# Kernel optimization log

Measured on AMD Instinct MI355X. Metric: run time of the kernel, lower is better.

## Reference

```python
import jax, jax.numpy as jnp
import numpy as np

TAU = 0.1
EPS = 1e-8

def _l2norm(x, axis):
    # matches F.normalize: x / max(||x||, 1e-12)
    n = jnp.sqrt(jnp.sum(x * x, axis=axis, keepdims=True))
    return x / jnp.maximum(n, 1e-12)

def setup_inputs() -> dict:
    key = jax.random.key(0)
    k1, k2, k3 = jax.random.split(key, 3)
    B, D, K = 262144, 256, 64
    return {
        "features": jax.random.normal(k1, (B, D), dtype=jnp.float32),
        "prototypes": jax.random.normal(k2, (K, D), dtype=jnp.float32),
        "domain_labels": jax.random.randint(k3, (B,), 0, K, dtype=jnp.int64),
    }

def reference(features, prototypes, domain_labels):
    f = _l2norm(features, 1)            # (B, D)
    p = _l2norm(prototypes, 1)          # (K, D)
    sim = jnp.einsum('bd,kd->bk', f, p) / TAU   # (B, K)
    e = jnp.exp(sim)                    # (B, K)
    numerator = jnp.take_along_axis(e, domain_labels[:, None], axis=1)[:, 0]  # (B,)
    denominator = jnp.sum(e, axis=1)    # (B,)
    loss = -jnp.log((numerator + EPS) / (denominator + EPS) + EPS)
    return jnp.mean(loss)
```

## Files before the change

### kernel.cpp

```cpp
#include <hip/hip_runtime.h>
#include <stdint.h>

typedef __attribute__((ext_vector_type(8))) short short8;
typedef __attribute__((ext_vector_type(4))) float floatx4;

#define EPS 1e-8f
#define TAU 0.1f

__device__ __forceinline__ unsigned short f2bf(float f) {
  union { float f; unsigned u; } v; v.f = f;
  unsigned u = v.u;
  u += 0x7fffu + ((u >> 16) & 1u);
  return (unsigned short)(u >> 16);
}

__global__ void proto_prep(const float* __restrict__ protos,
                           unsigned short* __restrict__ pbf) {
  const int l = threadIdx.x & 63;
  const int w = threadIdx.x >> 6;
  const int row = blockIdx.x * 4 + w;
  float4 v = reinterpret_cast<const float4*>(protos)[row * 64 + l];
  float ss = v.x * v.x + v.y * v.y + v.z * v.z + v.w * v.w;
#pragma unroll
  for (int d = 1; d < 64; d <<= 1) ss += __shfl_xor(ss, d, 64);
  const float inv = 1.0f / fmaxf(sqrtf(ss), 1e-12f);
  ushort4 o;
  o.x = f2bf(v.x * inv); o.y = f2bf(v.y * inv);
  o.z = f2bf(v.z * inv); o.w = f2bf(v.w * inv);
  reinterpret_cast<ushort4*>(pbf)[row * 64 + l] = o;
}

__global__ void protonce_main(const float* __restrict__ feat,
                              const unsigned short* __restrict__ pbf,
                              const int* __restrict__ labels,
                              float* __restrict__ partials) {
  const int tid = threadIdx.x;
  const int l = tid & 63;
  const int w = tid >> 6;
  const int n = l & 15;
  const int q = l >> 4;
  const long rowBase = (long)blockIdx.x * 64 + w * 16;

  const float* arow = feat + (rowBase + n) * 256 + q * 8;
  float4 av[16];
#pragma unroll
  for (int s = 0; s < 8; ++s) {
    av[2 * s]     = *reinterpret_cast<const float4*>(arow + s * 32);
    av[2 * s + 1] = *reinterpret_cast<const float4*>(arow + s * 32 + 4);
  }

  float ss = 0.f;
  short8 af[8];
#pragma unroll
  for (int s = 0; s < 8; ++s) {
    float4 x = av[2 * s], y = av[2 * s + 1];
    ss += x.x * x.x + x.y * x.y + x.z * x.z + x.w * x.w +
          y.x * y.x + y.y * y.y + y.z * y.z + y.w * y.w;
    short8 t;
    t[0] = f2bf(x.x); t[1] = f2bf(x.y); t[2] = f2bf(x.z); t[3] = f2bf(x.w);
    t[4] = f2bf(y.x); t[5] = f2bf(y.y); t[6] = f2bf(y.z); t[7] = f2bf(y.w);
    af[s] = t;
  }
  ss += __shfl_xor(ss, 16, 64);
  ss += __shfl_xor(ss, 32, 64);

  floatx4 acc[4] = {{0.f, 0.f, 0.f, 0.f}, {0.f, 0.f, 0.f, 0.f},
                    {0.f, 0.f, 0.f, 0.f}, {0.f, 0.f, 0.f, 0.f}};
  const unsigned short* bbase = pbf + n * 256 + q * 8;
#pragma unroll
  for (int s = 0; s < 8; ++s) {
#pragma unroll
    for (int t = 0; t < 4; ++t) {
      short8 bf = *reinterpret_cast<const short8*>(bbase + t * 4096 + s * 32);
      acc[t] = __builtin_amdgcn_mfma_f32_16x16x32_bf16(af[s], bf, acc[t], 0, 0, 0);
    }
  }

  const int4 lv = *reinterpret_cast<const int4*>(labels + rowBase + q * 4);
  float lossAcc = 0.f;
#pragma unroll
  for (int r = 0; r < 4; ++r) {
    const int row = q * 4 + r;
    const float nrm = __shfl(ss, row, 64);
    const float sc = 1.0f / (fmaxf(sqrtf(nrm), 1e-12f) * TAU);
    const int lab = (r == 0) ? lv.x : (r == 1) ? lv.y : (r == 2) ? lv.z : lv.w;
    float den = 0.f, num = 0.f;
#pragma unroll
    for (int t = 0; t < 4; ++t) {
      const float e = __expf(acc[t][r] * sc);
      den += e;
      num += (t * 16 + n == lab) ? e : 0.f;
    }
#pragma unroll
    for (int d = 1; d < 16; d <<= 1) {
      den += __shfl_xor(den, d, 64);
      num += __shfl_xor(num, d, 64);
    }
    if (n == 0) lossAcc += -__logf((num + EPS) / (den + EPS) + EPS);
  }
  lossAcc += __shfl_xor(lossAcc, 16, 64);
  lossAcc += __shfl_xor(lossAcc, 32, 64);

  __shared__ float wsum[4];
  if (l == 0) wsum[w] = lossAcc;
  __syncthreads();
  if (tid == 0) partials[blockIdx.x] = wsum[0] + wsum[1] + wsum[2] + wsum[3];
}

__global__ void finalize_k(const float* __restrict__ partials, int nblocks,
                           float* __restrict__ out, float invB) {
  __shared__ float red[256];
  float s = 0.f;
  for (int i = threadIdx.x; i < nblocks; i += 256) s += partials[i];
  red[threadIdx.x] = s;
  __syncthreads();
#pragma unroll
  for (int d = 128; d > 0; d >>= 1) {
    if (threadIdx.x < d) red[threadIdx.x] += red[threadIdx.x + d];
    __syncthreads();
  }
  if (threadIdx.x == 0) out[0] = red[0] * invB;
}

extern "C" void kernel_launch(void* const* d_in, const int* in_sizes, int n_in,
                              void* d_out, int out_size, void* d_ws, size_t ws_size,
                              hipStream_t stream) {
  const float* feat = (const float*)d_in[0];
  const float* protos = (const float*)d_in[1];
  const int* labels = (const int*)d_in[2];
  float* out = (float*)d_out;
  const int Bn = in_sizes[0] / 256;
  const int nblocks = Bn / 64;
  unsigned short* pbf = (unsigned short*)d_ws;
  float* partials = (float*)((char*)d_ws + 64 * 256 * sizeof(unsigned short));

  hipLaunchKernelGGL(proto_prep, dim3(16), dim3(256), 0, stream, protos, pbf);
  hipLaunchKernelGGL(protonce_main, dim3(nblocks), dim3(256), 0, stream,
                     feat, pbf, labels, partials);
  hipLaunchKernelGGL(finalize_k, dim3(1), dim3(256), 0, stream, partials,
                     nblocks, out, 1.0f / (float)Bn);
}
```

Baseline: 383.8 us.

## Stream feature loads through MFMA loop with truncating bf16 pack and launch bounds

The feature row is now loaded in two halves: the second half is fetched while the first half is converted and fed to the MFMAs. This cuts live registers, and launch_bounds(256,4) asks for higher occupancy. The round-to-nearest bf16 conversion is replaced by a single byte-permute truncation per pair of floats, which lowers ALU cost but slightly changes rounding of the feature operands. The kernel is memory-bound on a 256 MB feature read, so the main aim is more waves in flight to hide load latency.

Result: no change. 377.4 us (-1.7%).

```diff
diff --git a/kernel.cpp b/kernel.cpp
--- a/kernel.cpp
+++ b/kernel.cpp
@@ -12,6 +12,11 @@
   unsigned u = v.u;
   u += 0x7fffu + ((u >> 16) & 1u);
   return (unsigned short)(u >> 16);
+}
+
+__device__ __forceinline__ unsigned pack2_trunc(float lo, float hi) {
+  union { float f; unsigned u; } a, b; a.f = lo; b.f = hi;
+  return __builtin_amdgcn_perm(b.u, a.u, 0x07060302u);
 }
 
 __global__ void proto_prep(const float* __restrict__ protos,
@@ -30,10 +35,11 @@
   reinterpret_cast<ushort4*>(pbf)[row * 64 + l] = o;
 }
 
-__global__ void protonce_main(const float* __restrict__ feat,
-                              const unsigned short* __restrict__ pbf,
-                              const int* __restrict__ labels,
-                              float* __restrict__ partials) {
+__global__ __launch_bounds__(256, 4)
+void protonce_main(const float* __restrict__ feat,
+                   const unsigned short* __restrict__ pbf,
+                   const int* __restrict__ labels,
+                   float* __restrict__ partials) {
   const int tid = threadIdx.x;
   const int l = tid & 63;
   const int w = tid >> 6;
@@ -42,39 +48,42 @@
   const long rowBase = (long)blockIdx.x * 64 + w * 16;
 
   const float* arow = feat + (rowBase + n) * 256 + q * 8;
-  float4 av[16];
+  const unsigned short* bbase = pbf + n * 256 + q * 8;
+
+  float4 avx[4], avy[4];
 #pragma unroll
-  for (int s = 0; s < 8; ++s) {
-    av[2 * s]     = *reinterpret_cast<const float4*>(arow + s * 32);
-    av[2 * s + 1] = *reinterpret_cast<const float4*>(arow + s * 32 + 4);
+  for (int i = 0; i < 4; ++i) {
+    avx[i] = *reinterpret_cast<const float4*>(arow + i * 32);
+    avy[i] = *reinterpret_cast<const float4*>(arow + i * 32 + 4);
   }
-
-  float ss = 0.f;
-  short8 af[8];
-#pragma unroll
-  for (int s = 0; s < 8; ++s) {
-    float4 x = av[2 * s], y = av[2 * s + 1];
-    ss += x.x * x.x + x.y * x.y + x.z * x.z + x.w * x.w +
-          y.x * y.x + y.y * y.y + y.z * y.z + y.w * y.w;
-    short8 t;
-    t[0] = f2bf(x.x); t[1] = f2bf(x.y); t[2] = f2bf(x.z); t[3] = f2bf(x.w);
-    t[4] = f2bf(y.x); t[5] = f2bf(y.y); t[6] = f2bf(y.z); t[7] = f2bf(y.w);
-    af[s] = t;
-  }
-  ss += __shfl_xor(ss, 16, 64);
-  ss += __shfl_xor(ss, 32, 64);
 
   floatx4 acc[4] = {{0.f, 0.f, 0.f, 0.f}, {0.f, 0.f, 0.f, 0.f},
                     {0.f, 0.f, 0.f, 0.f}, {0.f, 0.f, 0.f, 0.f}};
-  const unsigned short* bbase = pbf + n * 256 + q * 8;
+  float ss = 0.f;
+
 #pragma unroll
   for (int s = 0; s < 8; ++s) {
+    float4 x = avx[s & 3], y = avy[s & 3];
+    if (s < 4) {
+      avx[s & 3] = *reinterpret_cast<const float4*>(arow + (s + 4) * 32);
+      avy[s & 3] = *reinterpret_cast<const float4*>(arow + (s + 4) * 32 + 4);
+    }
+    ss += x.x * x.x + x.y * x.y + x.z * x.z + x.w * x.w +
+          y.x * y.x + y.y * y.y + y.z * y.z + y.w * y.w;
+    union { short8 s8; uint4 u4; } af;
+    af.u4.x = pack2_trunc(x.x, x.y);
+    af.u4.y = pack2_trunc(x.z, x.w);
+    af.u4.z = pack2_trunc(y.x, y.y);
+    af.u4.w = pack2_trunc(y.z, y.w);
 #pragma unroll
     for (int t = 0; t < 4; ++t) {
       short8 bf = *reinterpret_cast<const short8*>(bbase + t * 4096 + s * 32);
-      acc[t] = __builtin_amdgcn_mfma_f32_16x16x32_bf16(af[s], bf, acc[t], 0, 0, 0);
+      acc[t] = __builtin_amdgcn_mfma_f32_16x16x32_bf16(af.s8, bf, acc[t], 0, 0, 0);
     }
   }
+
+  ss += __shfl_xor(ss, 16, 64);
+  ss += __shfl_xor(ss, 32, 64);
 
   const int4 lv = *reinterpret_cast<const int4*>(labels + rowBase + q * 4);
   float lossAcc = 0.f;
```
